# Performance work log

Hardware: AMD Instinct MI355X
Metric: run time of the kernel (lower is better)

The kernel has to match this reference:

```python
import jax, jax.numpy as jnp
import numpy as np
from jax import lax

B, D, CIN, COUT, N = 4, 64, 128, 256, 200000
D2 = D // 2
LEAK = 0.333   # scn LeakyReLU / BatchNormLeakyReLU default leakiness
EPS = 1e-4     # scn BatchNorm default eps


def setup_inputs() -> dict:
    key = jax.random.key(0)
    k1, k2, k3, k4, k5 = jax.random.split(key, 5)
    features = jax.random.normal(k1, (N, CIN), dtype=jnp.float32)
    coords = jax.random.randint(k2, (N, 3), 0, D, dtype=jnp.int32)
    batch_idx = jax.random.randint(k3, (N,), 0, B, dtype=jnp.int32)
    W = jax.random.normal(k4, (2, 2, 2, CIN, COUT), dtype=jnp.float32) * 0.05
    bias = jax.random.normal(k5, (COUT,), dtype=jnp.float32) * 0.05
    gamma = jnp.ones((COUT,), dtype=jnp.float32)
    beta = jnp.zeros((COUT,), dtype=jnp.float32)
    return {"features": features, "coords": coords, "batch_idx": batch_idx,
            "W": W, "bias": bias, "gamma": gamma, "beta": beta}


def reference(features, coords, batch_idx, W, bias, gamma, beta):
    # Scatter sparse points into a dense voxel grid [B, D, D, D, CIN]
    dense = jnp.zeros((B, D, D, D, CIN), features.dtype).at[
        batch_idx, coords[:, 0], coords[:, 1], coords[:, 2]].add(features)
    # Active output sites: any active input voxel in the 2x2x2 block
    occ = jnp.zeros((B, D, D, D), bool).at[
        batch_idx, coords[:, 0], coords[:, 1], coords[:, 2]].set(True)
    mask = occ.reshape(B, D2, 2, D2, 2, D2, 2).any(axis=(2, 4, 6))  # [B,D2,D2,D2]
    m = mask[..., None].astype(features.dtype)

    # Stride-2, kernel-2 conv (non-overlapping blocks) == SCN sparse conv here
    out = lax.conv_general_dilated(
        dense, W, window_strides=(2, 2, 2), padding='VALID',
        dimension_numbers=('NDHWC', 'DHWIO', 'NDHWC'))  # [B,D2,D2,D2,COUT]
    out = (out + bias) * m  # bias only at active sites; inactive sites zero

    # BatchNorm statistics over ACTIVE output sites only
    cnt = jnp.sum(m)
    mean = jnp.sum(out, axis=(0, 1, 2, 3)) / cnt           # out already masked
    var = jnp.sum(((out - mean) ** 2) * m, axis=(0, 1, 2, 3)) / cnt
    xhat = (out - mean) * lax.rsqrt(var + EPS) * gamma + beta
    act = jnp.where(xhat >= 0, xhat, LEAK * xhat)
    return act * m
```

## Files before the change

### kernel.cpp

```cpp
#include <hip/hip_runtime.h>
#include <stdint.h>

#define N_PTS 200000
#define SITES 131072
#define CINC  128
#define COUTC 256
#define KTOT  1024
#define LEAK  0.333f
#define EPSbn 1e-4f

typedef __attribute__((ext_vector_type(8))) short bf16x8;
typedef __attribute__((ext_vector_type(4))) float f32x4;


__device__ __forceinline__ unsigned short f2bf(float f) {
  union { float f; unsigned u; } un; un.f = f;
  unsigned u = un.u;
  u += 0x7fffu + ((u >> 16) & 1u);
  return (unsigned short)(u >> 16);
}

__device__ __forceinline__ void gload_lds16(const void* g, void* l) {
  __builtin_amdgcn_global_load_lds(
      (__attribute__((address_space(1))) void*)(g),
      (__attribute__((address_space(3))) void*)(l), 16, 0, 0);
}


__global__ void wcvt_k(const float* __restrict__ W, unsigned short* __restrict__ WT) {
  int i = blockIdx.x * 256 + threadIdx.x;
  int cout = i >> 10, k = i & 1023;
  WT[i] = f2bf(W[k * COUTC + cout]);
}


__global__ void scatter_k(const float* __restrict__ feat, const int* __restrict__ coords,
                          const int* __restrict__ bidx, unsigned short* __restrict__ grid,
                          unsigned char* __restrict__ occ) {
  int p = blockIdx.x * 4 + (threadIdx.x >> 6);
  int l = threadIdx.x & 63;
  if (p >= N_PTS) return;
  int b = bidx[p];
  int x = coords[p * 3 + 0], y = coords[p * 3 + 1], z = coords[p * 3 + 2];
  int osite = b * 32768 + (((x >> 1) * 32 + (y >> 1)) << 5) + (z >> 1);
  int sub = ((x & 1) << 2) | ((y & 1) << 1) | (z & 1);
  if (l == 0) occ[osite] = 1;
  float2 v = reinterpret_cast<const float2*>(feat)[p * 64 + l];
  unsigned pk = ((unsigned)f2bf(v.y) << 16) | (unsigned)f2bf(v.x);
  unsigned short* dst = grid + (((size_t)osite * 8 + sub) << 7) + (l << 1);
  asm volatile("global_atomic_pk_add_bf16 %0, %1, off"
               :: "v"((unsigned long long)(uintptr_t)dst), "v"(pk) : "memory");
}


__global__ __launch_bounds__(512, 1) void conv_k(
    const unsigned short* __restrict__ gridA, const unsigned short* __restrict__ WT,
    const unsigned char* __restrict__ occ, const float* __restrict__ bias,
    float* __restrict__ out, float* __restrict__ gsum, float* __restrict__ gsumsq) {
  __shared__ __align__(16) char lds[49152];
  char* Alds = lds;
  char* Blds = lds + 16384;

  const int tid = threadIdx.x;
  const int lane = tid & 63;
  const int wid = tid >> 6;
  const int wm = wid >> 2, wn = wid & 3;
  const int mt = blockIdx.x;

  const char* Ab = (const char*)(gridA + (size_t)mt * 128 * KTOT);
  const char* Bb = (const char*)WT;

  f32x4 acc[4][4];
#pragma unroll
  for (int m = 0; m < 4; ++m)
#pragma unroll
    for (int n = 0; n < 4; ++n) acc[m][n] = (f32x4){0.f, 0.f, 0.f, 0.f};

  for (int t = 0; t < 16; ++t) {
#pragma unroll
    for (int i = 0; i < 2; ++i) {
      int s = tid + i * 512;
      int row = s >> 3, c = s & 7;
      gload_lds16(Ab + row * 2048 + t * 128 + ((c ^ (row & 7)) << 4),
                  Alds + (s << 4));
    }
#pragma unroll
    for (int i = 0; i < 4; ++i) {
      int s = tid + i * 512;
      int row = s >> 3, c = s & 7;
      gload_lds16(Bb + row * 2048 + t * 128 + ((c ^ (row & 7)) << 4),
                  Blds + (s << 4));
    }
    __syncthreads();
#pragma unroll
    for (int ks = 0; ks < 2; ++ks) {
      bf16x8 af[4], bfr[4];
#pragma unroll
      for (int m = 0; m < 4; ++m) {
        int row = wm * 64 + m * 16 + (lane & 15);
        int bc = ((ks * 4 + (lane >> 4)) ^ (row & 7)) << 4;
        af[m] = *(const bf16x8*)(Alds + row * 128 + bc);
      }
#pragma unroll
      for (int n = 0; n < 4; ++n) {
        int row = wn * 64 + n * 16 + (lane & 15);
        int bc = ((ks * 4 + (lane >> 4)) ^ (row & 7)) << 4;
        bfr[n] = *(const bf16x8*)(Blds + row * 128 + bc);
      }
#pragma unroll
      for (int m = 0; m < 4; ++m)
#pragma unroll
        for (int n = 0; n < 4; ++n)
          acc[m][n] = __builtin_amdgcn_mfma_f32_16x16x32_bf16(af[m], bfr[n], acc[m][n], 0, 0, 0);
    }
    __syncthreads();
  }

  const int colb = wn * 64 + (lane & 15);
  const int rowb = wm * 64 + ((lane >> 4) << 2);
  float msk[16];
#pragma unroll
  for (int m = 0; m < 4; ++m)
#pragma unroll
    for (int j = 0; j < 4; ++j) {
      int site = mt * 128 + rowb + m * 16 + j;
      msk[m * 4 + j] = occ[site] ? 1.0f : 0.0f;
    }
  float s[4] = {0.f, 0.f, 0.f, 0.f}, ss[4] = {0.f, 0.f, 0.f, 0.f};
#pragma unroll
  for (int n = 0; n < 4; ++n) {
    int cout = colb + n * 16;
    float bv = bias[cout];
#pragma unroll
    for (int m = 0; m < 4; ++m)
#pragma unroll
      for (int j = 0; j < 4; ++j) {
        int site = mt * 128 + rowb + m * 16 + j;
        float v = (acc[m][n][j] + bv) * msk[m * 4 + j];
        out[(size_t)site * COUTC + cout] = v;
        s[n] += v; ss[n] += v * v;
      }
  }
#pragma unroll
  for (int n = 0; n < 4; ++n) {
    float a = s[n], b = ss[n];
    a += __shfl_xor(a, 16); a += __shfl_xor(a, 32);
    b += __shfl_xor(b, 16); b += __shfl_xor(b, 32);
    if (lane < 16) {
      atomicAdd(&gsum[colb + n * 16], a);
      atomicAdd(&gsumsq[colb + n * 16], b);
    }
  }
}


__global__ void stats_k(const unsigned char* __restrict__ occ,
                        const float* __restrict__ gsum, const float* __restrict__ gsumsq,
                        const float* __restrict__ gamma, const float* __restrict__ beta,
                        float* __restrict__ scsh) {
  __shared__ float red[4];
  int tid = threadIdx.x;
  const uint4* o4 = (const uint4*)occ;
  unsigned c = 0;
  for (int i = tid; i < SITES / 16; i += 256) {
    uint4 u = o4[i];
    c += __popc(u.x & 0x01010101u) + __popc(u.y & 0x01010101u)
       + __popc(u.z & 0x01010101u) + __popc(u.w & 0x01010101u);
  }
  float cf = (float)c;
  for (int off = 32; off > 0; off >>= 1) cf += __shfl_down(cf, off);
  if ((tid & 63) == 0) red[tid >> 6] = cf;
  __syncthreads();
  float cnt = red[0] + red[1] + red[2] + red[3];
  float mean = gsum[tid] / cnt;
  float var = gsumsq[tid] / cnt - mean * mean;
  float sc = rsqrtf(var + EPSbn) * gamma[tid];
  scsh[tid] = sc;
  scsh[256 + tid] = beta[tid] - mean * sc;
}


__global__ void bn_k(float* __restrict__ out, const unsigned char* __restrict__ occ,
                     const float* __restrict__ scsh) {
  const int total = SITES * 64;
  int stride = gridDim.x * blockDim.x;
  for (int i = blockIdx.x * blockDim.x + threadIdx.x; i < total; i += stride) {
    float4 v = reinterpret_cast<float4*>(out)[i];
    float4 r;
    if (occ[i >> 6]) {
      int c4 = (i & 63) << 2;
      float s0 = scsh[c4], s1 = scsh[c4 + 1], s2 = scsh[c4 + 2], s3 = scsh[c4 + 3];
      float h0 = scsh[256 + c4], h1 = scsh[257 + c4], h2 = scsh[258 + c4], h3 = scsh[259 + c4];
      r.x = fmaf(v.x, s0, h0); if (r.x < 0.f) r.x *= LEAK;
      r.y = fmaf(v.y, s1, h1); if (r.y < 0.f) r.y *= LEAK;
      r.z = fmaf(v.z, s2, h2); if (r.z < 0.f) r.z *= LEAK;
      r.w = fmaf(v.w, s3, h3); if (r.w < 0.f) r.w *= LEAK;
    } else {
      r.x = r.y = r.z = r.w = 0.f;
    }
    reinterpret_cast<float4*>(out)[i] = r;
  }
}


extern "C" void kernel_launch(void* const* d_in, const int* in_sizes, int n_in,
                              void* d_out, int out_size, void* d_ws, size_t ws_size,
                              hipStream_t stream) {
  const float* feat   = (const float*)d_in[0];
  const int*   coords = (const int*)d_in[1];
  const int*   bidx   = (const int*)d_in[2];
  const float* W      = (const float*)d_in[3];
  const float* bias   = (const float*)d_in[4];
  const float* gamma  = (const float*)d_in[5];
  const float* beta   = (const float*)d_in[6];
  float* out = (float*)d_out;

  char* ws = (char*)d_ws;
  unsigned short* grid = (unsigned short*)ws;
  unsigned short* WT   = (unsigned short*)(ws + 268435456);
  unsigned char*  occ  = (unsigned char*)(ws + 268959744);
  float*          st   = (float*)(ws + 269090816);

  hipMemsetAsync(grid, 0, 268435456, stream);
  hipMemsetAsync(ws + 268959744, 0, 131072 + 2048, stream);

  wcvt_k   <<<1024,  256, 0, stream>>>(W, WT);
  scatter_k<<<50000, 256, 0, stream>>>(feat, coords, bidx, grid, occ);
  conv_k   <<<1024,  512, 0, stream>>>(grid, WT, occ, bias, out, st, st + 256);
  stats_k  <<<1,     256, 0, stream>>>(occ, st, st + 256, gamma, beta, st + 512);
  bn_k     <<<2048,  256, 0, stream>>>(out, occ, st + 512);
}
```

Baseline: 438.8 us.

## Replace dense grid scatter-GEMM with per-point sub-position GEMM and atomic accumulation

Instead of scattering features into a 256MB dense bf16 voxel grid and running a dense GEMM over all output sites, points are bucketed by their 2x2x2 sub-position. Each bucket runs a gathered GEMM against the matching weight slice and bf16-atomically adds results into a 64MB per-site accumulator. The bias is dropped because batch-norm mean subtraction cancels it. Statistics move to a separate multi-block reduction over the accumulator. This removes the large memset and the dense-grid traffic, at the cost of bf16 atomic accumulation precision and atomic contention.

Result: slower. 933.5 us (+112.8%).

```diff
diff --git a/kernel.cpp b/kernel.cpp
--- a/kernel.cpp
+++ b/kernel.cpp
@@ -3,9 +3,7 @@
 
 #define N_PTS 200000
 #define SITES 131072
-#define CINC  128
 #define COUTC 256
-#define KTOT  1024
 #define LEAK  0.333f
 #define EPSbn 1e-4f
 
@@ -20,12 +18,22 @@
   return (unsigned short)(u >> 16);
 }
 
+__device__ __forceinline__ float bf2f(unsigned short u) {
+  union { unsigned u; float f; } x; x.u = ((unsigned)u) << 16; return x.f;
+}
+
 __device__ __forceinline__ void gload_lds16(const void* g, void* l) {
   __builtin_amdgcn_global_load_lds(
       (__attribute__((address_space(1))) void*)(g),
       (__attribute__((address_space(3))) void*)(l), 16, 0, 0);
 }
 
+__device__ __forceinline__ void pk_atomic(unsigned short* dst, float lo, float hi) {
+  unsigned pk = ((unsigned)f2bf(hi) << 16) | (unsigned)f2bf(lo);
+  asm volatile("global_atomic_pk_add_bf16 %0, %1, off"
+               :: "v"((unsigned long long)(uintptr_t)dst), "v"(pk) : "memory");
+}
+
 
 __global__ void wcvt_k(const float* __restrict__ W, unsigned short* __restrict__ WT) {
   int i = blockIdx.x * 256 + threadIdx.x;
@@ -34,41 +42,69 @@
 }
 
 
-__global__ void scatter_k(const float* __restrict__ feat, const int* __restrict__ coords,
-                          const int* __restrict__ bidx, unsigned short* __restrict__ grid,
-                          unsigned char* __restrict__ occ) {
-  int p = blockIdx.x * 4 + (threadIdx.x >> 6);
-  int l = threadIdx.x & 63;
-  if (p >= N_PTS) return;
-  int b = bidx[p];
-  int x = coords[p * 3 + 0], y = coords[p * 3 + 1], z = coords[p * 3 + 2];
-  int osite = b * 32768 + (((x >> 1) * 32 + (y >> 1)) << 5) + (z >> 1);
+__global__ void fcvt_k(const float* __restrict__ feat, unsigned short* __restrict__ featb) {
+  int i = blockIdx.x * 256 + threadIdx.x;
+  const float4* f4 = (const float4*)feat;
+  float4 a = f4[i * 2], b = f4[i * 2 + 1];
+  union { unsigned short u[8]; uint4 v; } r;
+  r.u[0] = f2bf(a.x); r.u[1] = f2bf(a.y); r.u[2] = f2bf(a.z); r.u[3] = f2bf(a.w);
+  r.u[4] = f2bf(b.x); r.u[5] = f2bf(b.y); r.u[6] = f2bf(b.z); r.u[7] = f2bf(b.w);
+  ((uint4*)featb)[i] = r.v;
+}
+
+
+__global__ void pprep_k(const int* __restrict__ coords, const int* __restrict__ bidx,
+                        unsigned char* __restrict__ occ, unsigned* __restrict__ psite,
+                        unsigned* __restrict__ plist, unsigned* __restrict__ cnt8) {
+  int p = blockIdx.x * 256 + threadIdx.x;
+  bool ok = p < N_PTS;
+  int b = 0, x = 0, y = 0, z = 0;
+  if (ok) { b = bidx[p]; x = coords[3 * p]; y = coords[3 * p + 1]; z = coords[3 * p + 2]; }
+  unsigned site = b * 32768 + ((x >> 1) << 10) + ((y >> 1) << 5) + (z >> 1);
   int sub = ((x & 1) << 2) | ((y & 1) << 1) | (z & 1);
-  if (l == 0) occ[osite] = 1;
-  float2 v = reinterpret_cast<const float2*>(feat)[p * 64 + l];
-  unsigned pk = ((unsigned)f2bf(v.y) << 16) | (unsigned)f2bf(v.x);
-  unsigned short* dst = grid + (((size_t)osite * 8 + sub) << 7) + (l << 1);
-  asm volatile("global_atomic_pk_add_bf16 %0, %1, off"
-               :: "v"((unsigned long long)(uintptr_t)dst), "v"(pk) : "memory");
-}
-
-
-__global__ __launch_bounds__(512, 1) void conv_k(
-    const unsigned short* __restrict__ gridA, const unsigned short* __restrict__ WT,
-    const unsigned char* __restrict__ occ, const float* __restrict__ bias,
-    float* __restrict__ out, float* __restrict__ gsum, float* __restrict__ gsumsq) {
+  if (ok) { occ[site] = 1; psite[p] = site; }
+  int lane = threadIdx.x & 63;
+  for (int s = 0; s < 8; ++s) {
+    unsigned long long m = __ballot(ok && sub == s);
+    if (m == 0ull) continue;
+    int n = __popcll(m);
+    int leader = __ffsll((long long)m) - 1;
+    unsigned base = 0;
+    if (lane == leader) base = atomicAdd(&cnt8[s], (unsigned)n);
+    base = (unsigned)__shfl((int)base, leader);
+    unsigned long long lt = m & ((lane == 63) ? 0x7fffffffffffffffull : ((1ull << lane) - 1ull));
+    if (ok && sub == s) plist[s * N_PTS + base + __popcll(lt)] = p;
+  }
+}
+
+
+__global__ __launch_bounds__(512, 1) void pgemm_k(
+    const unsigned short* __restrict__ featb, const unsigned short* __restrict__ WT,
+    const unsigned* __restrict__ plist, const unsigned* __restrict__ cnt8,
+    const unsigned* __restrict__ psite, unsigned short* __restrict__ accum) {
+  const int sub = blockIdx.y;
+  const unsigned cnt = cnt8[sub];
+  const unsigned tile0 = blockIdx.x * 128u;
+  if (tile0 >= cnt) return;
+
   __shared__ __align__(16) char lds[49152];
-  char* Alds = lds;
-  char* Blds = lds + 16384;
-
-  const int tid = threadIdx.x;
-  const int lane = tid & 63;
-  const int wid = tid >> 6;
-  const int wm = wid >> 2, wn = wid & 3;
-  const int mt = blockIdx.x;
-
-  const char* Ab = (const char*)(gridA + (size_t)mt * 128 * KTOT);
-  const char* Bb = (const char*)WT;
+  __shared__ unsigned pids[128];
+  __shared__ unsigned sites[128];
+  char* Wlds = lds;
+  char* Flds = lds + 32768;
+
+  const int tid = threadIdx.x, lane = tid & 63, wid = tid >> 6;
+  const int wm = wid >> 1, wn = wid & 1;
+
+  if (tid < 128) {
+    unsigned g = tile0 + tid;
+    unsigned pid = (g < cnt) ? plist[sub * N_PTS + g] : 0u;
+    pids[tid] = pid;
+    sites[tid] = psite[pid];
+  }
+  __syncthreads();
+
+  const char* Wb = (const char*)WT + sub * 256;
 
   f32x4 acc[4][4];
 #pragma unroll
@@ -76,20 +112,19 @@
 #pragma unroll
     for (int n = 0; n < 4; ++n) acc[m][n] = (f32x4){0.f, 0.f, 0.f, 0.f};
 
-  for (int t = 0; t < 16; ++t) {
+  for (int t = 0; t < 2; ++t) {
+#pragma unroll
+    for (int i = 0; i < 4; ++i) {
+      int s = tid + i * 512;
+      int row = s >> 3, c = s & 7;
+      gload_lds16(Wb + row * 2048 + t * 128 + ((c ^ (row & 7)) << 4), Wlds + (s << 4));
+    }
 #pragma unroll
     for (int i = 0; i < 2; ++i) {
       int s = tid + i * 512;
       int row = s >> 3, c = s & 7;
-      gload_lds16(Ab + row * 2048 + t * 128 + ((c ^ (row & 7)) << 4),
-                  Alds + (s << 4));
-    }
-#pragma unroll
-    for (int i = 0; i < 4; ++i) {
-      int s = tid + i * 512;
-      int row = s >> 3, c = s & 7;
-      gload_lds16(Bb + row * 2048 + t * 128 + ((c ^ (row & 7)) << 4),
-                  Blds + (s << 4));
+      gload_lds16((const char*)featb + (size_t)pids[row] * 256 + t * 128 + ((c ^ (row & 7)) << 4),
+                  Flds + (s << 4));
     }
     __syncthreads();
 #pragma unroll
@@ -99,13 +134,13 @@
       for (int m = 0; m < 4; ++m) {
         int row = wm * 64 + m * 16 + (lane & 15);
         int bc = ((ks * 4 + (lane >> 4)) ^ (row & 7)) << 4;
-        af[m] = *(const bf16x8*)(Alds + row * 128 + bc);
+        af[m] = *(const bf16x8*)(Wlds + row * 128 + bc);
       }
 #pragma unroll
       for (int n = 0; n < 4; ++n) {
         int row = wn * 64 + n * 16 + (lane & 15);
         int bc = ((ks * 4 + (lane >> 4)) ^ (row & 7)) << 4;
-        bfr[n] = *(const bf16x8*)(Blds + row * 128 + bc);
+        bfr[n] = *(const bf16x8*)(Flds + row * 128 + bc);
       }
 #pragma unroll
       for (int m = 0; m < 4; ++m)
@@ -116,89 +151,81 @@
     __syncthreads();
   }
 
-  const int colb = wn * 64 + (lane & 15);
-  const int rowb = wm * 64 + ((lane >> 4) << 2);
-  float msk[16];
-#pragma unroll
-  for (int m = 0; m < 4; ++m)
-#pragma unroll
-    for (int j = 0; j < 4; ++j) {
-      int site = mt * 128 + rowb + m * 16 + j;
-      msk[m * 4 + j] = occ[site] ? 1.0f : 0.0f;
-    }
-  float s[4] = {0.f, 0.f, 0.f, 0.f}, ss[4] = {0.f, 0.f, 0.f, 0.f};
 #pragma unroll
   for (int n = 0; n < 4; ++n) {
-    int cout = colb + n * 16;
-    float bv = bias[cout];
-#pragma unroll
-    for (int m = 0; m < 4; ++m)
-#pragma unroll
-      for (int j = 0; j < 4; ++j) {
-        int site = mt * 128 + rowb + m * 16 + j;
-        float v = (acc[m][n][j] + bv) * msk[m * 4 + j];
-        out[(size_t)site * COUTC + cout] = v;
-        s[n] += v; ss[n] += v * v;
-      }
-  }
-#pragma unroll
-  for (int n = 0; n < 4; ++n) {
-    float a = s[n], b = ss[n];
-    a += __shfl_xor(a, 16); a += __shfl_xor(a, 32);
-    b += __shfl_xor(b, 16); b += __shfl_xor(b, 32);
-    if (lane < 16) {
-      atomicAdd(&gsum[colb + n * 16], a);
-      atomicAdd(&gsumsq[colb + n * 16], b);
-    }
-  }
-}
-
-
-__global__ void stats_k(const unsigned char* __restrict__ occ,
-                        const float* __restrict__ gsum, const float* __restrict__ gsumsq,
-                        const float* __restrict__ gamma, const float* __restrict__ beta,
-                        float* __restrict__ scsh) {
-  __shared__ float red[4];
-  int tid = threadIdx.x;
-  const uint4* o4 = (const uint4*)occ;
-  unsigned c = 0;
-  for (int i = tid; i < SITES / 16; i += 256) {
-    uint4 u = o4[i];
-    c += __popc(u.x & 0x01010101u) + __popc(u.y & 0x01010101u)
-       + __popc(u.z & 0x01010101u) + __popc(u.w & 0x01010101u);
-  }
-  float cf = (float)c;
-  for (int off = 32; off > 0; off >>= 1) cf += __shfl_down(cf, off);
-  if ((tid & 63) == 0) red[tid >> 6] = cf;
+    int pt = wn * 64 + n * 16 + (lane & 15);
+    if (tile0 + pt >= cnt) continue;
+    unsigned site = sites[pt];
+    unsigned short* rowp = accum + (size_t)site * 256;
+#pragma unroll
+    for (int m = 0; m < 4; ++m) {
+      int cout0 = wm * 64 + m * 16 + ((lane >> 4) << 2);
+      pk_atomic(rowp + cout0,     acc[m][n][0], acc[m][n][1]);
+      pk_atomic(rowp + cout0 + 2, acc[m][n][2], acc[m][n][3]);
+    }
+  }
+}
+
+
+__global__ void stats_k(const unsigned short* __restrict__ accum,
+                        const unsigned char* __restrict__ occ, float* __restrict__ st) {
+  __shared__ float sA[4][256], sB[4][256];
+  int tid = threadIdx.x, lane = tid & 63, w = tid >> 6;
+  int base = blockIdx.x * 256;
+  float sv[4] = {0, 0, 0, 0}, svv[4] = {0, 0, 0, 0};
+  for (int r = w; r < 256; r += 4) {
+    const ushort4* row = (const ushort4*)(accum + (size_t)(base + r) * 256);
+    ushort4 u = row[lane];
+    float v0 = bf2f(u.x), v1 = bf2f(u.y), v2 = bf2f(u.z), v3 = bf2f(u.w);
+    sv[0] += v0; svv[0] += v0 * v0;
+    sv[1] += v1; svv[1] += v1 * v1;
+    sv[2] += v2; svv[2] += v2 * v2;
+    sv[3] += v3; svv[3] += v3 * v3;
+  }
+#pragma unroll
+  for (int k = 0; k < 4; ++k) { sA[w][lane * 4 + k] = sv[k]; sB[w][lane * 4 + k] = svv[k]; }
   __syncthreads();
-  float cnt = red[0] + red[1] + red[2] + red[3];
-  float mean = gsum[tid] / cnt;
-  float var = gsumsq[tid] / cnt - mean * mean;
-  float sc = rsqrtf(var + EPSbn) * gamma[tid];
-  scsh[tid] = sc;
-  scsh[256 + tid] = beta[tid] - mean * sc;
-}
-
-
-__global__ void bn_k(float* __restrict__ out, const unsigned char* __restrict__ occ,
-                     const float* __restrict__ scsh) {
+  float a = sA[0][tid] + sA[1][tid] + sA[2][tid] + sA[3][tid];
+  float b = sB[0][tid] + sB[1][tid] + sB[2][tid] + sB[3][tid];
+  atomicAdd(&st[tid], a);
+  atomicAdd(&st[256 + tid], b);
+  float c = occ[base + tid] ? 1.0f : 0.0f;
+  for (int off = 32; off > 0; off >>= 1) c += __shfl_down(c, off);
+  if (lane == 0) atomicAdd(&st[512], c);
+}
+
+__global__ void fin_k(const float* __restrict__ gamma, const float* __restrict__ beta,
+                      float* __restrict__ st) {
+  int t = threadIdx.x;
+  float cnt = st[512];
+  float mv = st[t] / cnt;
+  float var = st[256 + t] / cnt - mv * mv;
+  float sc = rsqrtf(var + EPSbn) * gamma[t];
+  st[1024 + t] = sc;
+  st[1280 + t] = beta[t] - mv * sc;
+}
+
+
+__global__ void bn_k(const unsigned short* __restrict__ accum,
+                     const unsigned char* __restrict__ occ,
+                     const float* __restrict__ st, float* __restrict__ out) {
+  const float* sc = st + 1024;
+  const float* sh = st + 1280;
   const int total = SITES * 64;
   int stride = gridDim.x * blockDim.x;
   for (int i = blockIdx.x * blockDim.x + threadIdx.x; i < total; i += stride) {
-    float4 v = reinterpret_cast<float4*>(out)[i];
     float4 r;
     if (occ[i >> 6]) {
       int c4 = (i & 63) << 2;
-      float s0 = scsh[c4], s1 = scsh[c4 + 1], s2 = scsh[c4 + 2], s3 = scsh[c4 + 3];
-      float h0 = scsh[256 + c4], h1 = scsh[257 + c4], h2 = scsh[258 + c4], h3 = scsh[259 + c4];
-      r.x = fmaf(v.x, s0, h0); if (r.x < 0.f) r.x *= LEAK;
-      r.y = fmaf(v.y, s1, h1); if (r.y < 0.f) r.y *= LEAK;
-      r.z = fmaf(v.z, s2, h2); if (r.z < 0.f) r.z *= LEAK;
-      r.w = fmaf(v.w, s3, h3); if (r.w < 0.f) r.w *= LEAK;
+      ushort4 u = ((const ushort4*)accum)[i];
+      r.x = fmaf(bf2f(u.x), sc[c4],     sh[c4]);     if (r.x < 0.f) r.x *= LEAK;
+      r.y = fmaf(bf2f(u.y), sc[c4 + 1], sh[c4 + 1]); if (r.y < 0.f) r.y *= LEAK;
+      r.z = fmaf(bf2f(u.z), sc[c4 + 2], sh[c4 + 2]); if (r.z < 0.f) r.z *= LEAK;
+      r.w = fmaf(bf2f(u.w), sc[c4 + 3], sh[c4 + 3]); if (r.w < 0.f) r.w *= LEAK;
     } else {
       r.x = r.y = r.z = r.w = 0.f;
     }
-    reinterpret_cast<float4*>(out)[i] = r;
+    ((float4*)out)[i] = r;
   }
 }
 
@@ -210,23 +237,28 @@
   const int*   coords = (const int*)d_in[1];
   const int*   bidx   = (const int*)d_in[2];
   const float* W      = (const float*)d_in[3];
-  const float* bias   = (const float*)d_in[4];
   const float* gamma  = (const float*)d_in[5];
   const float* beta   = (const float*)d_in[6];
   float* out = (float*)d_out;
 
   char* ws = (char*)d_ws;
-  unsigned short* grid = (unsigned short*)ws;
-  unsigned short* WT   = (unsigned short*)(ws + 268435456);
-  unsigned char*  occ  = (unsigned char*)(ws + 268959744);
-  float*          st   = (float*)(ws + 269090816);
-
-  hipMemsetAsync(grid, 0, 268435456, stream);
-  hipMemsetAsync(ws + 268959744, 0, 131072 + 2048, stream);
-
-  wcvt_k   <<<1024,  256, 0, stream>>>(W, WT);
-  scatter_k<<<50000, 256, 0, stream>>>(feat, coords, bidx, grid, occ);
-  conv_k   <<<1024,  512, 0, stream>>>(grid, WT, occ, bias, out, st, st + 256);
-  stats_k  <<<1,     256, 0, stream>>>(occ, st, st + 256, gamma, beta, st + 512);
-  bn_k     <<<2048,  256, 0, stream>>>(out, occ, st + 512);
-}
+  unsigned short* accum = (unsigned short*)ws;
+  unsigned char*  occ   = (unsigned char*)(ws + 67108864);
+  unsigned*       cnt8  = (unsigned*)(ws + 67239936);
+  float*          st    = (float*)(ws + 67239968);
+  unsigned short* featb = (unsigned short*)(ws + 67248160);
+  unsigned short* WT    = (unsigned short*)(ws + 118448160);
+  unsigned*       psite = (unsigned*)(ws + 118972448);
+  unsigned*       plist = (unsigned*)(ws + 119772448);
+
+  hipMemsetAsync(accum, 0, 67108864, stream);
+  hipMemsetAsync(occ, 0, 131072 + 32 + 8192, stream);
+
+  wcvt_k <<<1024,  256, 0, stream>>>(W, WT);
+  fcvt_k <<<12500, 256, 0, stream>>>(feat, featb);
+  pprep_k<<<782,   256, 0, stream>>>(coords, bidx, occ, psite, plist, cnt8);
+  pgemm_k<<<dim3(1563, 8, 1), 512, 0, stream>>>(featb, WT, plist, cnt8, psite, accum);
+  stats_k<<<512,   256, 0, stream>>>(accum, occ, st);
+  fin_k  <<<1,     256, 0, stream>>>(gamma, beta, st);
+  bn_k   <<<2048,  256, 0, stream>>>(accum, occ, st, out);
+}
```

## Replace dense voxel grid scatter with sorted compact gather and indirect conv loads

Applied to the files above, without the earlier changes.

The dense 268MB bf16 grid memset and per-point atomic scatter are replaced by a counting-sort pipeline: per-site histogram and sub-voxel mask, prefix scans, then point placement. A gather kernel sums the features of each active sub-voxel into a compact buffer. The conv kernel loads A rows indirectly through the mask and rank, pointing empty sub-voxels at a zero page. The conv bias is dropped because BatchNorm's mean subtraction cancels it, and the pre-BN tensor is stored in bf16 to halve traffic, at some cost in precision.

Result: slower. 487.1 us (+11.0%).

```diff
diff --git a/kernel.cpp b/kernel.cpp
--- a/kernel.cpp
+++ b/kernel.cpp
@@ -3,9 +3,7 @@
 
 #define N_PTS 200000
 #define SITES 131072
-#define CINC  128
 #define COUTC 256
-#define KTOT  1024
 #define LEAK  0.333f
 #define EPSbn 1e-4f
 
@@ -20,6 +18,10 @@
   return (unsigned short)(u >> 16);
 }
 
+__device__ __forceinline__ float bf2f(unsigned short u) {
+  union { unsigned u; float f; } x; x.u = ((unsigned)u) << 16; return x.f;
+}
+
 __device__ __forceinline__ void gload_lds16(const void* g, void* l) {
   __builtin_amdgcn_global_load_lds(
       (__attribute__((address_space(1))) void*)(g),
@@ -34,29 +36,122 @@
 }
 
 
-__global__ void scatter_k(const float* __restrict__ feat, const int* __restrict__ coords,
-                          const int* __restrict__ bidx, unsigned short* __restrict__ grid,
-                          unsigned char* __restrict__ occ) {
-  int p = blockIdx.x * 4 + (threadIdx.x >> 6);
-  int l = threadIdx.x & 63;
+__global__ void pprep_k(const int* __restrict__ coords, const int* __restrict__ bidx,
+                        unsigned* __restrict__ hist, unsigned* __restrict__ submask,
+                        unsigned* __restrict__ psitesub) {
+  int p = blockIdx.x * 256 + threadIdx.x;
   if (p >= N_PTS) return;
   int b = bidx[p];
-  int x = coords[p * 3 + 0], y = coords[p * 3 + 1], z = coords[p * 3 + 2];
-  int osite = b * 32768 + (((x >> 1) * 32 + (y >> 1)) << 5) + (z >> 1);
-  int sub = ((x & 1) << 2) | ((y & 1) << 1) | (z & 1);
-  if (l == 0) occ[osite] = 1;
-  float2 v = reinterpret_cast<const float2*>(feat)[p * 64 + l];
-  unsigned pk = ((unsigned)f2bf(v.y) << 16) | (unsigned)f2bf(v.x);
-  unsigned short* dst = grid + (((size_t)osite * 8 + sub) << 7) + (l << 1);
-  asm volatile("global_atomic_pk_add_bf16 %0, %1, off"
-               :: "v"((unsigned long long)(uintptr_t)dst), "v"(pk) : "memory");
+  int x = coords[3 * p], y = coords[3 * p + 1], z = coords[3 * p + 2];
+  unsigned site = b * 32768 + ((x >> 1) << 10) + ((y >> 1) << 5) + (z >> 1);
+  unsigned sub = ((x & 1) << 2) | ((y & 1) << 1) | (z & 1);
+  psitesub[p] = site * 8 + sub;
+  atomicAdd(&hist[site], 1u);
+  atomicOr(&submask[site], 1u << sub);
+}
+
+
+__global__ void scan1_k(const unsigned* __restrict__ hist, const unsigned* __restrict__ submask,
+                        unsigned* __restrict__ offs, unsigned* __restrict__ srank,
+                        unsigned* __restrict__ bsum1, unsigned* __restrict__ bsum2) {
+  __shared__ unsigned w1[4], w2[4];
+  int t = threadIdx.x, lane = t & 63, w = t >> 6;
+  int i = blockIdx.x * 256 + t;
+  unsigned v1 = hist[i], v2 = (unsigned)__popc(submask[i]);
+  unsigned s1 = v1, s2 = v2;
+  for (int d = 1; d < 64; d <<= 1) {
+    unsigned n1 = (unsigned)__shfl_up((int)s1, d);
+    unsigned n2 = (unsigned)__shfl_up((int)s2, d);
+    if (lane >= d) { s1 += n1; s2 += n2; }
+  }
+  if (lane == 63) { w1[w] = s1; w2[w] = s2; }
+  __syncthreads();
+  unsigned o1 = 0, o2 = 0;
+  for (int k = 0; k < w; ++k) { o1 += w1[k]; o2 += w2[k]; }
+  offs[i]  = o1 + s1 - v1;
+  srank[i] = o2 + s2 - v2;
+  if (t == 255) { bsum1[blockIdx.x] = o1 + s1; bsum2[blockIdx.x] = o2 + s2; }
+}
+
+__global__ void scan2_k(const unsigned* __restrict__ bsum1, const unsigned* __restrict__ bsum2,
+                        unsigned* __restrict__ boff1, unsigned* __restrict__ boff2) {
+  __shared__ unsigned w1[8], w2[8];
+  int t = threadIdx.x, lane = t & 63, w = t >> 6;
+  unsigned v1 = bsum1[t], v2 = bsum2[t], s1 = v1, s2 = v2;
+  for (int d = 1; d < 64; d <<= 1) {
+    unsigned n1 = (unsigned)__shfl_up((int)s1, d);
+    unsigned n2 = (unsigned)__shfl_up((int)s2, d);
+    if (lane >= d) { s1 += n1; s2 += n2; }
+  }
+  if (lane == 63) { w1[w] = s1; w2[w] = s2; }
+  __syncthreads();
+  unsigned o1 = 0, o2 = 0;
+  for (int k = 0; k < w; ++k) { o1 += w1[k]; o2 += w2[k]; }
+  boff1[t] = o1 + s1 - v1;
+  boff2[t] = o2 + s2 - v2;
+}
+
+__global__ void scan3_k(unsigned* __restrict__ offs, unsigned* __restrict__ srank,
+                        unsigned* __restrict__ cursor,
+                        const unsigned* __restrict__ boff1, const unsigned* __restrict__ boff2,
+                        const unsigned* __restrict__ submask, float* __restrict__ st) {
+  int i = blockIdx.x * 256 + threadIdx.x;
+  unsigned o = offs[i] + boff1[blockIdx.x];
+  offs[i] = o; cursor[i] = o;
+  srank[i] += boff2[blockIdx.x];
+  float c = submask[i] ? 1.0f : 0.0f;
+  for (int off = 32; off > 0; off >>= 1) c += __shfl_down(c, off);
+  if ((threadIdx.x & 63) == 0) atomicAdd(&st[512], c);
+}
+
+__global__ void place_k(const unsigned* __restrict__ psitesub, unsigned* __restrict__ cursor,
+                        unsigned* __restrict__ plist) {
+  int p = blockIdx.x * 256 + threadIdx.x;
+  if (p >= N_PTS) return;
+  unsigned ss = psitesub[p];
+  unsigned pos = atomicAdd(&cursor[ss >> 3], 1u);
+  plist[pos] = ((unsigned)p << 3) | (ss & 7);
+}
+
+
+__global__ __launch_bounds__(512) void gather_k(
+    const float* __restrict__ feat, const unsigned* __restrict__ hist,
+    const unsigned* __restrict__ offs, const unsigned* __restrict__ plist,
+    const unsigned* __restrict__ submask, const unsigned* __restrict__ srank,
+    unsigned* __restrict__ gc) {
+  int site = blockIdx.x * 8 + (threadIdx.x >> 6);
+  int lane = threadIdx.x & 63;
+  unsigned n = hist[site];
+  if (!n) return;
+  unsigned o = offs[site];
+  unsigned msk = submask[site], base = srank[site];
+  for (unsigned i = 0; i < n; ++i) {
+    unsigned e = plist[o + i];
+    unsigned sub = e & 7;
+    bool owner = true;
+    for (unsigned j = 0; j < i; ++j)
+      if ((plist[o + j] & 7) == sub) { owner = false; break; }
+    if (!owner) continue;
+    float2 a = ((const float2*)feat)[(size_t)(e >> 3) * 64 + lane];
+    for (unsigned j = i + 1; j < n; ++j) {
+      unsigned e2 = plist[o + j];
+      if ((e2 & 7) == sub) {
+        float2 b2 = ((const float2*)feat)[(size_t)(e2 >> 3) * 64 + lane];
+        a.x += b2.x; a.y += b2.y;
+      }
+    }
+    unsigned vr = base + __popc(msk & ((1u << sub) - 1u));
+    unsigned pk = ((unsigned)f2bf(a.y) << 16) | (unsigned)f2bf(a.x);
+    gc[(size_t)vr * 64 + lane] = pk;
+  }
 }
 
 
 __global__ __launch_bounds__(512, 1) void conv_k(
-    const unsigned short* __restrict__ gridA, const unsigned short* __restrict__ WT,
-    const unsigned char* __restrict__ occ, const float* __restrict__ bias,
-    float* __restrict__ out, float* __restrict__ gsum, float* __restrict__ gsumsq) {
+    const unsigned char* __restrict__ gc, const unsigned short* __restrict__ WT,
+    const unsigned* __restrict__ submask, const unsigned* __restrict__ srank,
+    const unsigned char* __restrict__ zp, unsigned short* __restrict__ accumb,
+    float* __restrict__ st) {
   __shared__ __align__(16) char lds[49152];
   char* Alds = lds;
   char* Blds = lds + 16384;
@@ -67,7 +162,10 @@
   const int wm = wid >> 2, wn = wid & 3;
   const int mt = blockIdx.x;
 
-  const char* Ab = (const char*)(gridA + (size_t)mt * 128 * KTOT);
+  const int s0 = tid,        row0 = s0 >> 3, c0 = s0 & 7;
+  const int s1 = tid + 512,  row1 = s1 >> 3, c1 = s1 & 7;
+  const unsigned m0 = submask[mt * 128 + row0], b0 = srank[mt * 128 + row0];
+  const unsigned m1 = submask[mt * 128 + row1], b1 = srank[mt * 128 + row1];
   const char* Bb = (const char*)WT;
 
   f32x4 acc[4][4];
@@ -77,19 +175,24 @@
     for (int n = 0; n < 4; ++n) acc[m][n] = (f32x4){0.f, 0.f, 0.f, 0.f};
 
   for (int t = 0; t < 16; ++t) {
-#pragma unroll
-    for (int i = 0; i < 2; ++i) {
-      int s = tid + i * 512;
-      int row = s >> 3, c = s & 7;
-      gload_lds16(Ab + row * 2048 + t * 128 + ((c ^ (row & 7)) << 4),
-                  Alds + (s << 4));
+    const int sub = t >> 1, half = (t & 1) * 128;
+    {
+      unsigned ok = (m0 >> sub) & 1u;
+      unsigned vr = b0 + __popc(m0 & ((1u << sub) - 1u));
+      const char* src = ok ? (const char*)gc + (size_t)vr * 256 : (const char*)zp;
+      gload_lds16(src + half + ((c0 ^ (row0 & 7)) << 4), Alds + (s0 << 4));
+    }
+    {
+      unsigned ok = (m1 >> sub) & 1u;
+      unsigned vr = b1 + __popc(m1 & ((1u << sub) - 1u));
+      const char* src = ok ? (const char*)gc + (size_t)vr * 256 : (const char*)zp;
+      gload_lds16(src + half + ((c1 ^ (row1 & 7)) << 4), Alds + (s1 << 4));
     }
 #pragma unroll
     for (int i = 0; i < 4; ++i) {
       int s = tid + i * 512;
       int row = s >> 3, c = s & 7;
-      gload_lds16(Bb + row * 2048 + t * 128 + ((c ^ (row & 7)) << 4),
-                  Blds + (s << 4));
+      gload_lds16(Bb + row * 2048 + t * 128 + ((c ^ (row & 7)) << 4), Blds + (s << 4));
     }
     __syncthreads();
 #pragma unroll
@@ -118,87 +221,73 @@
 
   const int colb = wn * 64 + (lane & 15);
   const int rowb = wm * 64 + ((lane >> 4) << 2);
-  float msk[16];
+  float mskv[16];
 #pragma unroll
   for (int m = 0; m < 4; ++m)
 #pragma unroll
     for (int j = 0; j < 4; ++j) {
       int site = mt * 128 + rowb + m * 16 + j;
-      msk[m * 4 + j] = occ[site] ? 1.0f : 0.0f;
-    }
-  float s[4] = {0.f, 0.f, 0.f, 0.f}, ss[4] = {0.f, 0.f, 0.f, 0.f};
+      mskv[m * 4 + j] = submask[site] ? 1.0f : 0.0f;
+    }
+  float sv[4] = {0.f, 0.f, 0.f, 0.f}, ssv[4] = {0.f, 0.f, 0.f, 0.f};
 #pragma unroll
   for (int n = 0; n < 4; ++n) {
     int cout = colb + n * 16;
-    float bv = bias[cout];
 #pragma unroll
     for (int m = 0; m < 4; ++m)
 #pragma unroll
       for (int j = 0; j < 4; ++j) {
         int site = mt * 128 + rowb + m * 16 + j;
-        float v = (acc[m][n][j] + bv) * msk[m * 4 + j];
-        out[(size_t)site * COUTC + cout] = v;
-        s[n] += v; ss[n] += v * v;
+        float v = acc[m][n][j] * mskv[m * 4 + j];
+        accumb[(size_t)site * 256 + cout] = f2bf(v);
+        sv[n] += v; ssv[n] += v * v;
       }
   }
 #pragma unroll
   for (int n = 0; n < 4; ++n) {
-    float a = s[n], b = ss[n];
+    float a = sv[n], b = ssv[n];
     a += __shfl_xor(a, 16); a += __shfl_xor(a, 32);
     b += __shfl_xor(b, 16); b += __shfl_xor(b, 32);
     if (lane < 16) {
-      atomicAdd(&gsum[colb + n * 16], a);
-      atomicAdd(&gsumsq[colb + n * 16], b);
-    }
-  }
-}
-
-
-__global__ void stats_k(const unsigned char* __restrict__ occ,
-                        const float* __restrict__ gsum, const float* __restrict__ gsumsq,
-                        const float* __restrict__ gamma, const float* __restrict__ beta,
-                        float* __restrict__ scsh) {
-  __shared__ float red[4];
-  int tid = threadIdx.x;
-  const uint4* o4 = (const uint4*)occ;
-  unsigned c = 0;
-  for (int i = tid; i < SITES / 16; i += 256) {
-    uint4 u = o4[i];
-    c += __popc(u.x & 0x01010101u) + __popc(u.y & 0x01010101u)
-       + __popc(u.z & 0x01010101u) + __popc(u.w & 0x01010101u);
-  }
-  float cf = (float)c;
-  for (int off = 32; off > 0; off >>= 1) cf += __shfl_down(cf, off);
-  if ((tid & 63) == 0) red[tid >> 6] = cf;
-  __syncthreads();
-  float cnt = red[0] + red[1] + red[2] + red[3];
-  float mean = gsum[tid] / cnt;
-  float var = gsumsq[tid] / cnt - mean * mean;
-  float sc = rsqrtf(var + EPSbn) * gamma[tid];
-  scsh[tid] = sc;
-  scsh[256 + tid] = beta[tid] - mean * sc;
-}
-
-
-__global__ void bn_k(float* __restrict__ out, const unsigned char* __restrict__ occ,
-                     const float* __restrict__ scsh) {
+      atomicAdd(&st[colb + n * 16], a);
+      atomicAdd(&st[256 + colb + n * 16], b);
+    }
+  }
+}
+
+
+__global__ void fin_k(const float* __restrict__ gamma, const float* __restrict__ beta,
+                      float* __restrict__ st) {
+  int t = threadIdx.x;
+  float cnt = st[512];
+  float mv = st[t] / cnt;
+  float var = st[256 + t] / cnt - mv * mv;
+  float sc = rsqrtf(var + EPSbn) * gamma[t];
+  st[1024 + t] = sc;
+  st[1280 + t] = beta[t] - mv * sc;
+}
+
+
+__global__ void bn_k(const unsigned short* __restrict__ accumb,
+                     const unsigned* __restrict__ submask,
+                     const float* __restrict__ st, float* __restrict__ out) {
+  const float* sc = st + 1024;
+  const float* sh = st + 1280;
   const int total = SITES * 64;
   int stride = gridDim.x * blockDim.x;
   for (int i = blockIdx.x * blockDim.x + threadIdx.x; i < total; i += stride) {
-    float4 v = reinterpret_cast<float4*>(out)[i];
     float4 r;
-    if (occ[i >> 6]) {
+    if (submask[i >> 6]) {
       int c4 = (i & 63) << 2;
-      float s0 = scsh[c4], s1 = scsh[c4 + 1], s2 = scsh[c4 + 2], s3 = scsh[c4 + 3];
-      float h0 = scsh[256 + c4], h1 = scsh[257 + c4], h2 = scsh[258 + c4], h3 = scsh[259 + c4];
-      r.x = fmaf(v.x, s0, h0); if (r.x < 0.f) r.x *= LEAK;
-      r.y = fmaf(v.y, s1, h1); if (r.y < 0.f) r.y *= LEAK;
-      r.z = fmaf(v.z, s2, h2); if (r.z < 0.f) r.z *= LEAK;
-      r.w = fmaf(v.w, s3, h3); if (r.w < 0.f) r.w *= LEAK;
+      ushort4 u = ((const ushort4*)accumb)[i];
+      r.x = fmaf(bf2f(u.x), sc[c4],     sh[c4]);     if (r.x < 0.f) r.x *= LEAK;
+      r.y = fmaf(bf2f(u.y), sc[c4 + 1], sh[c4 + 1]); if (r.y < 0.f) r.y *= LEAK;
+      r.z = fmaf(bf2f(u.z), sc[c4 + 2], sh[c4 + 2]); if (r.z < 0.f) r.z *= LEAK;
+      r.w = fmaf(bf2f(u.w), sc[c4 + 3], sh[c4 + 3]); if (r.w < 0.f) r.w *= LEAK;
     } else {
       r.x = r.y = r.z = r.w = 0.f;
     }
-    reinterpret_cast<float4*>(out)[i] = r;
+    ((float4*)out)[i] = r;
   }
 }
 
@@ -210,23 +299,39 @@
   const int*   coords = (const int*)d_in[1];
   const int*   bidx   = (const int*)d_in[2];
   const float* W      = (const float*)d_in[3];
-  const float* bias   = (const float*)d_in[4];
   const float* gamma  = (const float*)d_in[5];
   const float* beta   = (const float*)d_in[6];
   float* out = (float*)d_out;
 
   char* ws = (char*)d_ws;
-  unsigned short* grid = (unsigned short*)ws;
-  unsigned short* WT   = (unsigned short*)(ws + 268435456);
-  unsigned char*  occ  = (unsigned char*)(ws + 268959744);
-  float*          st   = (float*)(ws + 269090816);
-
-  hipMemsetAsync(grid, 0, 268435456, stream);
-  hipMemsetAsync(ws + 268959744, 0, 131072 + 2048, stream);
-
-  wcvt_k   <<<1024,  256, 0, stream>>>(W, WT);
-  scatter_k<<<50000, 256, 0, stream>>>(feat, coords, bidx, grid, occ);
-  conv_k   <<<1024,  512, 0, stream>>>(grid, WT, occ, bias, out, st, st + 256);
-  stats_k  <<<1,     256, 0, stream>>>(occ, st, st + 256, gamma, beta, st + 512);
-  bn_k     <<<2048,  256, 0, stream>>>(out, occ, st + 512);
-}
+  unsigned*       gc      = (unsigned*)ws;
+  unsigned short* accumb  = (unsigned short*)(ws + 51200000);
+  unsigned short* WT      = (unsigned short*)(ws + 118308864);
+  unsigned*       hist    = (unsigned*)(ws + 118833152);
+  unsigned*       submask = (unsigned*)(ws + 119357440);
+  unsigned*       offs    = (unsigned*)(ws + 119881728);
+  unsigned*       cursor  = (unsigned*)(ws + 120406016);
+  unsigned*       srank   = (unsigned*)(ws + 120930304);
+  unsigned*       bsum1   = (unsigned*)(ws + 121454592);
+  unsigned*       bsum2   = (unsigned*)(ws + 121456640);
+  unsigned*       boff1   = (unsigned*)(ws + 121458688);
+  unsigned*       boff2   = (unsigned*)(ws + 121460736);
+  unsigned*       psitesub= (unsigned*)(ws + 121462784);
+  unsigned*       plist   = (unsigned*)(ws + 122262784);
+  float*          st      = (float*)(ws + 123062784);
+  unsigned char*  zp      = (unsigned char*)(ws + 123070976);
+
+  hipMemsetAsync(hist, 0, 1048576, stream);
+  hipMemsetAsync(st, 0, 10240, stream);
+
+  wcvt_k  <<<1024,  256, 0, stream>>>(W, WT);
+  pprep_k <<<782,   256, 0, stream>>>(coords, bidx, hist, submask, psitesub);
+  scan1_k <<<512,   256, 0, stream>>>(hist, submask, offs, srank, bsum1, bsum2);
+  scan2_k <<<1,     512, 0, stream>>>(bsum1, bsum2, boff1, boff2);
+  scan3_k <<<512,   256, 0, stream>>>(offs, srank, cursor, boff1, boff2, submask, st);
+  place_k <<<782,   256, 0, stream>>>(psitesub, cursor, plist);
+  gather_k<<<16384, 512, 0, stream>>>(feat, hist, offs, plist, submask, srank, gc);
+  conv_k  <<<1024,  512, 0, stream>>>((const unsigned char*)gc, WT, submask, srank, zp, accumb, st);
+  fin_k   <<<1,     256, 0, stream>>>(gamma, beta, st);
+  bn_k    <<<2048,  256, 0, stream>>>(accumb, submask, st, out);
+}
```
